# Optimization experiments

Hardware: AMD Instinct MI355X
Metric: run time of the kernel (lower is better)

## Reference

```python
import jax, jax.numpy as jnp
import numpy as np

B = 4; C = 3; IMG = 256; P = 16; HP = 16; HW = 256
DIM = 512; DEPTH = 6; HEADS = 8; DH = 64
NS = 50; SH = 4; SDH = 64; ITERS = 3; RPD = 128; FF = 2048; N = NS + HW


def _ln(x, g, b):
    m = jnp.mean(x, -1, keepdims=True)
    v = jnp.var(x, -1, keepdims=True)
    return (x - m) * jax.lax.rsqrt(v + 1e-5) * g + b


def _rms(x, g):
    # lucidrains RMSNorm: F.normalize(x, dim=-1) * sqrt(dim) * gamma
    n = jnp.linalg.norm(x, axis=-1, keepdims=True)
    return x / jnp.maximum(n, 1e-12) * (DIM ** 0.5) * g


def setup_inputs() -> dict:
    key = jax.random.key(0)
    ks = iter(jax.random.split(key, 64))
    def W(*s):
        return jax.random.normal(next(ks), s, jnp.float32) * 0.02
    SI = SH * SDH
    d = {}
    d['images'] = jax.random.normal(next(ks), (B, C, IMG, IMG), jnp.float32)
    d['slot_noise'] = jax.random.normal(next(ks), (B, NS, DIM), jnp.float32)
    d['patch_w'] = W(C * P * P, DIM); d['patch_b'] = jnp.zeros((DIM,))
    d['hpos'] = W(HP, DIM); d['wpos'] = W(HP, DIM)
    d['rp_w1'] = W(2, RPD); d['rp_b1'] = jnp.zeros((RPD,))
    d['rp_w2'] = W(RPD, RPD); d['rp_b2'] = jnp.zeros((RPD,))
    d['rp_w3'] = W(RPD, HEADS); d['rp_b3'] = jnp.zeros((HEADS,))
    d['slots_mu'] = W(1, 1, DIM); d['slots_logsigma'] = jnp.zeros((1, 1, DIM))
    d['sa_ln_in_g'] = jnp.ones((DIM,)); d['sa_ln_in_b'] = jnp.zeros((DIM,))
    d['sa_ln_sl_g'] = jnp.ones((DIM,)); d['sa_ln_sl_b'] = jnp.zeros((DIM,))
    d['sa_wq'] = W(DIM, SI); d['sa_bq'] = jnp.zeros((SI,))
    d['sa_wk'] = W(DIM, SI); d['sa_bk'] = jnp.zeros((SI,))
    d['sa_wv'] = W(DIM, SI); d['sa_bv'] = jnp.zeros((SI,))
    d['sa_wo'] = W(SI, DIM); d['sa_bo'] = jnp.zeros((DIM,))
    d['gru_wih'] = W(DIM, 3 * DIM); d['gru_whh'] = W(DIM, 3 * DIM)
    d['gru_bih'] = jnp.zeros((3 * DIM,)); d['gru_bhh'] = jnp.zeros((3 * DIM,))
    d['sa_ln_ff_g'] = jnp.ones((DIM,)); d['sa_ln_ff_b'] = jnp.zeros((DIM,))
    d['sa_mlp_w1'] = W(DIM, DIM); d['sa_mlp_b1'] = jnp.zeros((DIM,))
    d['sa_mlp_w2'] = W(DIM, DIM); d['sa_mlp_b2'] = jnp.zeros((DIM,))
    d['s2c_w'] = W(DIM, 2); d['s2c_b'] = jnp.zeros((2,))
    d['attn_g'] = jnp.ones((DEPTH, DIM))
    d['wq'] = W(DEPTH, DIM, HEADS * DH); d['wk'] = W(DEPTH, DIM, HEADS * DH)
    d['wv'] = W(DEPTH, DIM, HEADS * DH); d['wo'] = W(DEPTH, HEADS * DH, DIM)
    d['ff_g'] = jnp.ones((DEPTH, DIM))
    d['ff_w1'] = W(DEPTH, DIM, FF); d['ff_b1'] = jnp.zeros((DEPTH, FF))
    d['ff_w2'] = W(DEPTH, FF, DIM); d['ff_b2'] = jnp.zeros((DEPTH, DIM))
    d['final_g'] = jnp.ones((DIM,))
    d['pred_w'] = W(DIM, DIM); d['pred_b'] = jnp.zeros((DIM,))
    return d


def reference(images, slot_noise, patch_w, patch_b, hpos, wpos,
              rp_w1, rp_b1, rp_w2, rp_b2, rp_w3, rp_b3,
              slots_mu, slots_logsigma, sa_ln_in_g, sa_ln_in_b, sa_ln_sl_g, sa_ln_sl_b,
              sa_wq, sa_bq, sa_wk, sa_bk, sa_wv, sa_bv, sa_wo, sa_bo,
              gru_wih, gru_whh, gru_bih, gru_bhh, sa_ln_ff_g, sa_ln_ff_b,
              sa_mlp_w1, sa_mlp_b1, sa_mlp_w2, sa_mlp_b2, s2c_w, s2c_b,
              attn_g, wq, wk, wv, wo, ff_g, ff_w1, ff_b1, ff_w2, ff_b2,
              final_g, pred_w, pred_b):
    b = images.shape[0]
    # patchify: b c (h p1) (w p2) -> b h w (p1 p2 c)
    x = images.reshape(b, C, HP, P, HP, P).transpose(0, 2, 4, 3, 5, 1).reshape(b, HP, HP, P * P * C)
    tokens = x @ patch_w + patch_b                     # [b, HP, HP, DIM]
    tokens = tokens + hpos[:, None, :] + wpos[None, :, :]
    tokens = tokens.reshape(b, HW, DIM)
    # --- multi-head slot attention ---
    inp = _ln(tokens, sa_ln_in_g, sa_ln_in_b)
    k = (inp @ sa_wk + sa_bk).reshape(b, HW, SH, SDH).transpose(0, 2, 1, 3)
    v = (inp @ sa_wv + sa_bv).reshape(b, HW, SH, SDH).transpose(0, 2, 1, 3)
    slots = slots_mu + jnp.exp(slots_logsigma) * slot_noise  # [b, NS, DIM]
    scale = SDH ** -0.5
    for _ in range(ITERS):
        prev = slots
        s = _ln(slots, sa_ln_sl_g, sa_ln_sl_b)
        q = (s @ sa_wq + sa_bq).reshape(b, NS, SH, SDH).transpose(0, 2, 1, 3)
        dots = jnp.einsum('bhid,bhjd->bhij', q, k) * scale     # [b, SH, NS, HW]
        attn = jax.nn.softmax(dots, axis=-2) + 1e-8            # softmax over slots
        attn = attn / jnp.sum(attn, -1, keepdims=True)         # weighted mean over inputs
        upd = jnp.einsum('bhij,bhjd->bhid', attn, v)
        upd = upd.transpose(0, 2, 1, 3).reshape(b, NS, SH * SDH) @ sa_wo + sa_bo
        # GRUCell(updates, prev_slots)
        gx = upd @ gru_wih + gru_bih
        gh = prev @ gru_whh + gru_bhh
        xr, xz, xn = jnp.split(gx, 3, -1)
        hr, hz, hn = jnp.split(gh, 3, -1)
        r = jax.nn.sigmoid(xr + hr)
        z = jax.nn.sigmoid(xz + hz)
        nn_ = jnp.tanh(xn + r * hn)
        slots = (1 - z) * nn_ + z * prev
        slots = slots + (jax.nn.relu(_ln(slots, sa_ln_ff_g, sa_ln_ff_b) @ sa_mlp_w1 + sa_mlp_b1) @ sa_mlp_w2 + sa_mlp_b2)
    objects = slots
    slot_coords = objects @ s2c_w + s2c_b              # [b, NS, 2]
    # --- relative position MLP bias (slots coords + patch grid) ---
    g = jnp.arange(HP, dtype=jnp.float32)
    grid = jnp.stack(jnp.meshgrid(g, g, indexing='ij'), -1).reshape(HW, 2)
    coords = jnp.concatenate([slot_coords, jnp.broadcast_to(grid, (b, HW, 2))], axis=1)  # [b, N, 2]
    rel = coords[:, :, None, :] - coords[:, None, :, :]   # [b, N, N, 2]
    hmid = jax.nn.silu(rel @ rp_w1 + rp_b1)
    hmid = jax.nn.silu(hmid @ rp_w2 + rp_b2)
    bias = jnp.transpose(hmid @ rp_w3 + rp_b3, (0, 3, 1, 2))  # [b, HEADS, N, N]
    # --- transformer with per-layer rel-pos bias ---
    x = jnp.concatenate([objects, tokens], axis=1)     # [b, N, DIM]
    ascale = DH ** -0.5
    for l in range(DEPTH):
        h = _rms(x, attn_g[l])
        qh = (h @ wq[l]).reshape(b, N, HEADS, DH).transpose(0, 2, 1, 3)
        kh = (h @ wk[l]).reshape(b, N, HEADS, DH).transpose(0, 2, 1, 3)
        vh = (h @ wv[l]).reshape(b, N, HEADS, DH).transpose(0, 2, 1, 3)
        sim = jnp.einsum('bhid,bhjd->bhij', qh, kh) * ascale + bias
        a = jax.nn.softmax(sim, -1)
        o = jnp.einsum('bhij,bhjd->bhid', a, vh).transpose(0, 2, 1, 3).reshape(b, N, HEADS * DH) @ wo[l]
        x = x + o
        h = _rms(x, ff_g[l])
        x = x + (jax.nn.gelu(h @ ff_w1[l] + ff_b1[l]) @ ff_w2[l] + ff_b2[l])
    x = _rms(x, final_g)
    return x[:, NS:] @ pred_w + pred_b                 # [b, HW, DIM]
```

## Files before the change

kernel.cpp:

```cpp
#include <hip/hip_runtime.h>
#include <hip/hip_bf16.h>

typedef __hip_bfloat16 bf16;
typedef short short8v __attribute__((ext_vector_type(8)));
typedef float float4v __attribute__((ext_vector_type(4)));

static __device__ __forceinline__ float b2f(bf16 x){ return __bfloat162float(x); }

static __device__ __forceinline__ float ldin(const void* p, size_t i, bool isbf) {
  return isbf ? b2f(((const bf16*)p)[i]) : ((const float*)p)[i];
}

static __device__ __forceinline__ unsigned short f2bu(float f) {
  bf16 h = __float2bfloat16(f);
  return *reinterpret_cast<unsigned short*>(&h);
}

#define CDIV(a,b) (((a)+(b)-1)/(b))

#define NB   4
#define NSL  50
#define HWT  256
#define NT   306
#define DIM  512
#define NH   8
#define FF   2048
#define RPP  28100
#define PCH  56200

static __device__ __forceinline__ void rp_decode(int q, int& i, int& j) {
  if (q < 15300) { i = q / NT; j = q % NT; }
  else { int r = q - 15300; i = NSL + r / NSL; j = r % NSL; }
}

__global__ void detect_k(const void* p, int* flag) {
  const unsigned short* u = (const unsigned short*)p;
  int t = threadIdx.x;
  int e = (u[t] >> 7) & 0xFF;
  __shared__ int anybad;
  if (t == 0) anybad = 0;
  __syncthreads();
  if (e >= 0x88) atomicOr(&anybad, 1);
  __syncthreads();
  if (t == 0) *flag = anybad ? 0 : 1;
}

struct WtArgs {
  const void* W[17];
  unsigned long long wto[17];
  int K[17], N[17];
  int base[18];
};

__global__ __launch_bounds__(256) void wtrans_all_k(WtArgs a, unsigned short* __restrict__ WT,
                                                    const int* __restrict__ flagp) {
  const bool isbf = *flagp != 0;
  int bid = blockIdx.x;
  int idx = 0;
#pragma unroll
  for (int i = 1; i < 17; ++i) if (bid >= a.base[i]) idx = i;
  int t0 = bid - a.base[idx];
  const int K = a.K[idx], N = a.N[idx];
  const int tilesN = N >> 6;
  const int perLayer = tilesN * (K >> 6);
  const int layer = t0 / perLayer, rem = t0 % perLayer;
  const int n0 = (rem % tilesN) * 64, k0 = (rem / tilesN) * 64;
  const void* W = a.W[idx];
  unsigned short* dst0 = WT + a.wto[idx];
  const size_t slice = (size_t)K * N * layer;

  __shared__ unsigned short S[64 * 72];
  int t = threadIdx.x;
  int kk = t >> 4, nn = (t & 15) * 4;
#pragma unroll
  for (int r = 0; r < 4; ++r) {
    int k = k0 + kk + r * 16;
    unsigned short v[4];
    if (isbf) {
      ushort4 u = *(const ushort4*)((const unsigned short*)W + slice + (size_t)k * N + n0 + nn);
      v[0]=u.x; v[1]=u.y; v[2]=u.z; v[3]=u.w;
    } else {
      float4 f = *(const float4*)((const float*)W + slice + (size_t)k * N + n0 + nn);
      v[0]=f2bu(f.x); v[1]=f2bu(f.y); v[2]=f2bu(f.z); v[3]=f2bu(f.w);
    }
#pragma unroll
    for (int i = 0; i < 4; ++i) S[(nn + i) * 72 + kk + r * 16] = v[i];
  }
  __syncthreads();
  int nr = t >> 2, kc = (t & 3) * 16;
  short8v s0 = *(const short8v*)&S[nr * 72 + kc];
  short8v s1 = *(const short8v*)&S[nr * 72 + kc + 8];
  unsigned short* dst = dst0 + slice + (size_t)(n0 + nr) * K + k0 + kc;
  *(short8v*)dst = s0;
  *(short8v*)(dst + 8) = s1;
}

static __device__ __forceinline__ void gemm_epi(
    float4v accv, int row0, int col,
    const void* __restrict__ bias, size_t boff,
    void* __restrict__ C, int oty,
    int M, int N, int kbeg,
    int act, int mode, int spec,
    const void* __restrict__ p0, const void* __restrict__ p1,
    bool isbf)
{
  float bv = (bias && kbeg == 0) ? ldin(bias, boff + col, isbf) : 0.f;
#pragma unroll
  for (int r = 0; r < 4; ++r) {
    int row = row0 + r;
    if (row >= M) continue;
    float v = accv[r] + bv;
    if (act == 1) v = fmaxf(v, 0.f);
    else if (act == 2) {
      float u = 0.7978845608028654f * (v + 0.044715f * v * v * v);
      v = 0.5f * v * (1.f + tanhf(u));
    } else if (act == 3) {
      v = v / (1.f + expf(-v));
    }
    if (spec == 2 && kbeg == 0) {
      int hh = (row >> 4) & 15, ww = row & 15;
      v += ldin(p0, hh * N + col, isbf) + ldin(p1, ww * N + col, isbf);
    }
    if (spec == 1) {
      int b_ = row / NT, n_ = row % NT;
      if (n_ >= NSL) {
        size_t oi = ((size_t)(b_ * HWT + (n_ - NSL))) * N + col;
        if (isbf) ((bf16*)C)[oi] = __float2bfloat16(v);
        else      ((float*)C)[oi] = v;
      }
    } else {
      size_t idx = (size_t)row * N + col;
      if (oty) ((bf16*)C)[idx] = __float2bfloat16(v);
      else {
        float* Cf = (float*)C;
        if (mode == 2) atomicAdd(&Cf[idx], v);
        else if (mode == 1) Cf[idx] += v;
        else Cf[idx] = v;
      }
    }
  }
}

#define LDK 72
static __device__ __forceinline__ void gemm_body2(
    const void* __restrict__ A, int aty,
    const unsigned short* __restrict__ WT,
    const void* __restrict__ bias, size_t boff,
    void* __restrict__ C, int oty,
    int M, int N, int K, int kbeg, int kend,
    int act, int mode, int spec,
    const void* __restrict__ p0, const void* __restrict__ p1,
    bool isbf)
{
  __shared__ unsigned short As[64 * LDK];
  __shared__ unsigned short Bs[64 * LDK];
  const int tid = threadIdx.x;
  const int lane = tid & 63, wave = tid >> 6;
  const int quad = lane >> 4, ti = lane & 15;
  const int wm = (wave & 1) * 32, wn = (wave >> 1) * 32;
  const int bm = blockIdx.y * 64, bn = blockIdx.x * 64;
  const int srow = tid >> 2, sch = (tid & 3) * 16;

  unsigned short ha[16], hb[16];
  const int gm = bm + srow;
  const bool aok = gm < M;
  const unsigned short* Abf = (const unsigned short*)A + (size_t)gm * K;
  const float*          Af  = (const float*)A + (size_t)gm * K;
  const unsigned short* Bp  = WT + (size_t)(bn + srow) * K;

  auto fetchA = [&](int k0) {
    if (aok) {
      if (aty) {
        const ushort4* ap = (const ushort4*)(Abf + k0 + sch);
#pragma unroll
        for (int i = 0; i < 4; ++i) {
          ushort4 u = ap[i];
          ha[i*4+0]=u.x; ha[i*4+1]=u.y; ha[i*4+2]=u.z; ha[i*4+3]=u.w;
        }
      } else {
        const float4* ap = (const float4*)(Af + k0 + sch);
#pragma unroll
        for (int i = 0; i < 4; ++i) {
          float4 f = ap[i];
          ha[i*4+0]=f2bu(f.x); ha[i*4+1]=f2bu(f.y); ha[i*4+2]=f2bu(f.z); ha[i*4+3]=f2bu(f.w);
        }
      }
    } else {
#pragma unroll
      for (int i = 0; i < 16; ++i) ha[i] = 0;
    }
  };
  auto fetchB = [&](int k0) {
    const ushort4* bp = (const ushort4*)(Bp + k0 + sch);
#pragma unroll
    for (int i = 0; i < 4; ++i) {
      ushort4 u = bp[i];
      hb[i*4+0]=u.x; hb[i*4+1]=u.y; hb[i*4+2]=u.z; hb[i*4+3]=u.w;
    }
  };

  float4v acc00 = {0,0,0,0}, acc01 = {0,0,0,0}, acc10 = {0,0,0,0}, acc11 = {0,0,0,0};
  fetchA(kbeg); fetchB(kbeg);
  for (int k0 = kbeg; k0 < kend; k0 += 64) {
    *(short8v*)&As[srow * LDK + sch]     = *(short8v*)ha;
    *(short8v*)&As[srow * LDK + sch + 8] = *(short8v*)(ha + 8);
    *(short8v*)&Bs[srow * LDK + sch]     = *(short8v*)hb;
    *(short8v*)&Bs[srow * LDK + sch + 8] = *(short8v*)(hb + 8);
    __syncthreads();
    if (k0 + 64 < kend) { fetchA(k0 + 64); fetchB(k0 + 64); }
#pragma unroll
    for (int ks = 0; ks < 2; ++ks) {
      short8v a0 = *reinterpret_cast<const short8v*>(&As[(wm + ti)      * LDK + ks * 32 + quad * 8]);
      short8v a1 = *reinterpret_cast<const short8v*>(&As[(wm + 16 + ti) * LDK + ks * 32 + quad * 8]);
      short8v b0 = *reinterpret_cast<const short8v*>(&Bs[(wn + ti)      * LDK + ks * 32 + quad * 8]);
      short8v b1 = *reinterpret_cast<const short8v*>(&Bs[(wn + 16 + ti) * LDK + ks * 32 + quad * 8]);
      acc00 = __builtin_amdgcn_mfma_f32_16x16x32_bf16(a0, b0, acc00, 0, 0, 0);
      acc01 = __builtin_amdgcn_mfma_f32_16x16x32_bf16(a0, b1, acc01, 0, 0, 0);
      acc10 = __builtin_amdgcn_mfma_f32_16x16x32_bf16(a1, b0, acc10, 0, 0, 0);
      acc11 = __builtin_amdgcn_mfma_f32_16x16x32_bf16(a1, b1, acc11, 0, 0, 0);
    }
    __syncthreads();
  }

  float4v accs[2][2] = {{acc00, acc01}, {acc10, acc11}};
#pragma unroll
  for (int mi = 0; mi < 2; ++mi)
#pragma unroll
    for (int ni = 0; ni < 2; ++ni)
      gemm_epi(accs[mi][ni], bm + wm + mi * 16 + quad * 4, bn + wn + ni * 16 + ti,
               bias, boff, C, oty, M, N, kbeg, act, mode, spec, p0, p1, isbf);
}

__global__ __launch_bounds__(256) void gemm_mfma(
    const void* A, int aty, const unsigned short* WT, size_t woff,
    const void* bias, size_t boff, void* C, int oty,
    int M, int N, int K, int act, int accum, int zsplit,
    int spec, const void* p0, const void* p1, const int* __restrict__ flagp)
{
  int ksz = K / zsplit;
  int kbeg = blockIdx.z * ksz;
  int mode = zsplit > 1 ? 2 : (accum ? 1 : 0);
  gemm_body2(A, aty, WT + woff, bias, boff, C, oty, M, N, K, kbeg, kbeg + ksz,
             act, mode, spec, p0, p1, *flagp != 0);
}

__global__ __launch_bounds__(256) void gemm_mfma_tri(
    const void* A, int aty, const unsigned short* WT, size_t o0, size_t o1, size_t o2,
    void* C0, void* C1, void* C2, int oty, int M, int N, int K,
    const int* __restrict__ flagp)
{
  size_t o = blockIdx.z == 0 ? o0 : (blockIdx.z == 1 ? o1 : o2);
  void* C = blockIdx.z == 0 ? C0 : (blockIdx.z == 1 ? C1 : C2);
  gemm_body2(A, aty, WT + o, nullptr, 0, C, oty, M, N, K, 0, K, 0, 0, 0,
             nullptr, nullptr, *flagp != 0);
}

__global__ __launch_bounds__(256) void gemm_mfma_duo(
    const void* A0, const void* A1, int aty, const unsigned short* WT, size_t o0, size_t o1,
    const void* bias0, const void* bias1, void* C0, void* C1, int oty,
    int M, int N, int K, const int* __restrict__ flagp)
{
  const void* A = blockIdx.z ? A1 : A0;
  size_t o = blockIdx.z ? o1 : o0;
  const void* bias = blockIdx.z ? bias1 : bias0;
  void* C = blockIdx.z ? C1 : C0;
  gemm_body2(A, aty, WT + o, bias, 0, C, oty, M, N, K, 0, K, 0, 0, 0,
             nullptr, nullptr, *flagp != 0);
}

__global__ void coords_k(const float* __restrict__ slots, const void* __restrict__ w,
                         const void* __restrict__ bv, float* __restrict__ coords,
                         const int* __restrict__ flagp) {
  const bool isbf = *flagp != 0;
  __shared__ float r0[256], r1[256];
  int blk = blockIdx.x, t = threadIdx.x;
  if (blk < 200) {
    int b = blk / 50, n = blk % 50;
    const float* x = slots + (size_t)blk * DIM;
    float v0 = x[t], v1 = x[t + 256];
    float a0 = v0 * ldin(w, 2 * t, isbf)     + v1 * ldin(w, 2 * (t + 256), isbf);
    float a1 = v0 * ldin(w, 2 * t + 1, isbf) + v1 * ldin(w, 2 * (t + 256) + 1, isbf);
    r0[t] = a0; r1[t] = a1;
    __syncthreads();
    for (int o = 128; o > 0; o >>= 1) {
      if (t < o) { r0[t] += r0[t + o]; r1[t] += r1[t + o]; }
      __syncthreads();
    }
    if (t == 0) {
      coords[((size_t)b * NT + n) * 2]     = r0[0] + ldin(bv, 0, isbf);
      coords[((size_t)b * NT + n) * 2 + 1] = r1[0] + ldin(bv, 1, isbf);
    }
  } else {
#pragma unroll
    for (int s = 0; s < 4; ++s) {
      int i = t + 256 * s;
      int b = i >> 8, tt = i & 255;
      coords[((size_t)b * NT + NSL + tt) * 2]     = (float)(tt >> 4);
      coords[((size_t)b * NT + NSL + tt) * 2 + 1] = (float)(tt & 15);
    }
  }
}

__global__ void patchify_k(const void* __restrict__ img, unsigned short* __restrict__ xp,
                           const int* __restrict__ flagp) {
  const bool isbf = *flagp != 0;
  int i = blockIdx.x * 256 + threadIdx.x;
  if (i >= NB * HWT * 768) return;
  int col = i % 768, row = i / 768;
  int c = col % 3, p2 = (col / 3) & 15, p1 = col / 48;
  int w = row & 15, h = (row >> 4) & 15, b = row >> 8;
  xp[i] = f2bu(ldin(img, (((size_t)(b * 3 + c) * 256 + h * 16 + p1) * 256) + w * 16 + p2, isbf));
}

__global__ void ln512_k(const float* __restrict__ X, const void* __restrict__ g,
                        const void* __restrict__ b, unsigned short* __restrict__ Y,
                        const int* __restrict__ flagp) {
  const bool isbf = *flagp != 0;
  int row = blockIdx.x, t = threadIdx.x;
  const float* x = X + (size_t)row * DIM;
  float v0 = x[t], v1 = x[t + 256];
  __shared__ float rs[256], rq[256];
  rs[t] = v0 + v1; rq[t] = v0 * v0 + v1 * v1;
  __syncthreads();
  for (int o = 128; o > 0; o >>= 1) {
    if (t < o) { rs[t] += rs[t + o]; rq[t] += rq[t + o]; }
    __syncthreads();
  }
  float mean = rs[0] * (1.f / 512.f);
  float var  = rq[0] * (1.f / 512.f) - mean * mean;
  float inv  = rsqrtf(var + 1e-5f);
  unsigned short* y = Y + (size_t)row * DIM;
  y[t]       = f2bu((v0 - mean) * inv * ldin(g, t, isbf)       + ldin(b, t, isbf));
  y[t + 256] = f2bu((v1 - mean) * inv * ldin(g, t + 256, isbf) + ldin(b, t + 256, isbf));
}

__global__ void rms512_k(const float* __restrict__ X, const void* __restrict__ g,
                         int goff, unsigned short* __restrict__ Y, const int* __restrict__ flagp) {
  const bool isbf = *flagp != 0;
  int row = blockIdx.x, t = threadIdx.x;
  const float* x = X + (size_t)row * DIM;
  float v0 = x[t], v1 = x[t + 256];
  __shared__ float rq[256];
  rq[t] = v0 * v0 + v1 * v1;
  __syncthreads();
  for (int o = 128; o > 0; o >>= 1) {
    if (t < o) rq[t] += rq[t + o];
    __syncthreads();
  }
  float nrm = sqrtf(rq[0]);
  float sc = 22.62741699796952f / fmaxf(nrm, 1e-12f);
  unsigned short* y = Y + (size_t)row * DIM;
  y[t]       = f2bu(v0 * sc * ldin(g, goff + t, isbf));
  y[t + 256] = f2bu(v1 * sc * ldin(g, goff + t + 256, isbf));
}

__global__ void slots_init_k(const void* __restrict__ mu, const void* __restrict__ ls,
                             const void* __restrict__ noise, float* __restrict__ slots,
                             const int* __restrict__ flagp) {
  const bool isbf = *flagp != 0;
  int i = blockIdx.x * 256 + threadIdx.x;
  if (i >= NB * NSL * DIM) return;
  int d = i & 511;
  slots[i] = ldin(mu, d, isbf) + expf(ldin(ls, d, isbf)) * ldin(noise, i, isbf);
}

__global__ void slot_dots_k(const float* __restrict__ q, const float* __restrict__ k,
                            float* __restrict__ dots) {
  int blk = blockIdx.x;
  int i = blk % 50, h = (blk / 50) & 3, b = blk / 200;
  int j = threadIdx.x;
  __shared__ float qs[64];
  if (threadIdx.x < 64) qs[threadIdx.x] = q[((size_t)(b * 50 + i)) * 256 + h * 64 + threadIdx.x];
  __syncthreads();
  const float* kr = k + ((size_t)(b * 256 + j)) * 256 + h * 64;
  float s = 0.f;
#pragma unroll 8
  for (int d = 0; d < 64; ++d) s = fmaf(qs[d], kr[d], s);
  dots[(((size_t)(b * 4 + h) * 50) + i) * 256 + j] = s * 0.125f;
}

__global__ void colsm_k(float* __restrict__ dots) {
  int idx = blockIdx.x * 256 + threadIdx.x;
  if (idx >= 4096) return;
  int j = idx & 255, bh = idx >> 8;
  float* base = dots + ((size_t)bh * NSL) * 256 + j;
  float v[NSL];
#pragma unroll
  for (int i = 0; i < NSL; ++i) v[i] = base[i * 256];
  float m = -1e30f;
#pragma unroll
  for (int i = 0; i < NSL; ++i) m = fmaxf(m, v[i]);
  float s = 0.f;
#pragma unroll
  for (int i = 0; i < NSL; ++i) { float e = __expf(v[i] - m); v[i] = e; s += e; }
  float inv = 1.f / s;
#pragma unroll
  for (int i = 0; i < NSL; ++i) base[i * 256] = fmaf(v[i], inv, 1e-8f);
}

__global__ void slot_upd_k(const float* __restrict__ attn, const float* __restrict__ v,
                           float* __restrict__ upd) {
  int bi = blockIdx.x;
  int b = bi / 50, i = bi % 50;
  int t = threadIdx.x, h = t >> 6, lane = t & 63;
  const float* arow = attn + ((size_t)((b * 4 + h) * 50) + i) * 256;
  float s4 = arow[lane] + arow[lane + 64] + arow[lane + 128] + arow[lane + 192];
#pragma unroll
  for (int o = 1; o < 64; o <<= 1) s4 += __shfl_xor(s4, o);
  float inv = 1.f / s4;
  float s = 0.f;
  for (int j = 0; j < 256; ++j) s = fmaf(arow[j], v[((size_t)(b * 256 + j)) * 256 + t], s);
  upd[(size_t)bi * 256 + t] = s * inv;
}

__global__ __launch_bounds__(256) void gruln_k(
    const float* __restrict__ gx, const float* __restrict__ gh,
    float* __restrict__ slots, const void* __restrict__ g, const void* __restrict__ bb,
    unsigned short* __restrict__ Y, const int* __restrict__ flagp) {
  const bool isbf = *flagp != 0;
  int row = blockIdx.x, t = threadIdx.x;
  size_t b3 = (size_t)row * 1536;
  float s01[2];
#pragma unroll
  for (int half = 0; half < 2; ++half) {
    int d = t + half * 256;
    float xr = gx[b3 + d], xz = gx[b3 + 512 + d], xn = gx[b3 + 1024 + d];
    float hr = gh[b3 + d], hz = gh[b3 + 512 + d], hn = gh[b3 + 1024 + d];
    float r = 1.f / (1.f + expf(-(xr + hr)));
    float z = 1.f / (1.f + expf(-(xz + hz)));
    float n = tanhf(xn + r * hn);
    float prev = slots[(size_t)row * DIM + d];
    s01[half] = (1.f - z) * n + z * prev;
    slots[(size_t)row * DIM + d] = s01[half];
  }
  __shared__ float rs[256], rq[256];
  rs[t] = s01[0] + s01[1];
  rq[t] = s01[0] * s01[0] + s01[1] * s01[1];
  __syncthreads();
  for (int o = 128; o > 0; o >>= 1) {
    if (t < o) { rs[t] += rs[t + o]; rq[t] += rq[t + o]; }
    __syncthreads();
  }
  float mean = rs[0] * (1.f / 512.f);
  float var  = rq[0] * (1.f / 512.f) - mean * mean;
  float inv  = rsqrtf(var + 1e-5f);
  unsigned short* y = Y + (size_t)row * DIM;
  y[t]       = f2bu((s01[0] - mean) * inv * ldin(g, t, isbf)       + ldin(bb, t, isbf));
  y[t + 256] = f2bu((s01[1] - mean) * inv * ldin(g, t + 256, isbf) + ldin(bb, t + 256, isbf));
}

__global__ void relpos_table_k(const void* w1, const void* b1, const void* w2,
                               const void* b2, const void* w3, const void* b3,
                               float* __restrict__ tab, const int* __restrict__ flagp) {
  const bool isbf = *flagp != 0;
  int blk = blockIdx.x;
  float r0 = (float)(blk / 31 - 15), r1 = (float)(blk % 31 - 15);
  int t = threadIdx.x;
  __shared__ float h1[128], h2[128];
  float a = fmaf(r0, ldin(w1, t, isbf), fmaf(r1, ldin(w1, 128 + t, isbf), ldin(b1, t, isbf)));
  h1[t] = a / (1.f + expf(-a));
  __syncthreads();
  float s = ldin(b2, t, isbf);
#pragma unroll 4
  for (int k = 0; k < 128; ++k) s = fmaf(h1[k], ldin(w2, k * 128 + t, isbf), s);
  h2[t] = s / (1.f + expf(-s));
  __syncthreads();
  if (t < 8) {
    float o = ldin(b3, t, isbf);
#pragma unroll 4
    for (int k = 0; k < 128; ++k) o = fmaf(h2[k], ldin(w3, k * 8 + t, isbf), o);
    tab[blk * 8 + t] = o;
  }
}

__global__ void rp_l1_k(const float* __restrict__ coords, const void* w1, const void* b1,
                        unsigned short* __restrict__ H, int pbase, int pcount,
                        const int* __restrict__ flagp) {
  const bool isbf = *flagp != 0;
  int idx = blockIdx.x * 256 + threadIdx.x;
  if (idx >= pcount * 128) return;
  int pl = idx >> 7, u = idx & 127;
  int p = pbase + pl;
  int q = p % RPP, bb = p / RPP;
  int ii, jj;
  rp_decode(q, ii, jj);
  float r0 = coords[(bb * NT + ii) * 2]     - coords[(bb * NT + jj) * 2];
  float r1 = coords[(bb * NT + ii) * 2 + 1] - coords[(bb * NT + jj) * 2 + 1];
  float a = fmaf(r0, ldin(w1, u, isbf), fmaf(r1, ldin(w1, 128 + u, isbf), ldin(b1, u, isbf)));
  H[(size_t)pl * 128 + u] = f2bu(a / (1.f + expf(-a)));
}

__global__ __launch_bounds__(256) void rp_l3_k(
    const unsigned short* __restrict__ H2, const void* w3, const void* b3,
    float* __restrict__ bias, int pbase, int pcount, const int* __restrict__ flagp) {
  const bool isbf = *flagp != 0;
  __shared__ float W3s[8 * 132];
  int t = threadIdx.x;
  for (int e = t; e < 1024; e += 256) {
    int k = e >> 3, hh = e & 7;
    W3s[hh * 132 + k] = ldin(w3, e, isbf);
  }
  __syncthreads();
  int pl = blockIdx.x * 32 + (t >> 3), hh = t & 7;
  if (pl >= pcount) return;
  int p = pbase + pl;
  int q = p % RPP, bb = p / RPP;
  int ii, jj;
  rp_decode(q, ii, jj);
  float s = ldin(b3, hh, isbf);
  const unsigned short* hrow = H2 + (size_t)pl * 128;
  const float* wrow = &W3s[hh * 132];
#pragma unroll 8
  for (int k4 = 0; k4 < 32; ++k4) {
    ushort4 h4 = *(const ushort4*)(hrow + k4 * 4);
    float4  w4 = *(const float4*)(wrow + k4 * 4);
    s = fmaf(b2f(*reinterpret_cast<bf16*>(&h4.x)), w4.x, s);
    s = fmaf(b2f(*reinterpret_cast<bf16*>(&h4.y)), w4.y, s);
    s = fmaf(b2f(*reinterpret_cast<bf16*>(&h4.z)), w4.z, s);
    s = fmaf(b2f(*reinterpret_cast<bf16*>(&h4.w)), w4.w, s);
  }
  bias[((size_t)(bb * NH + hh) * NT + ii) * NT + jj] = s;
}

__global__ void build_x_k(const float* __restrict__ slots, const float* __restrict__ tok,
                          float* __restrict__ x) {
  int i = blockIdx.x * 256 + threadIdx.x;
  if (i >= NB * NT * DIM) return;
  int d = i & 511, n = (i >> 9) % NT, b = i / (NT * DIM);
  x[i] = (n < NSL) ? slots[((size_t)(b * NSL + n)) * DIM + d]
                   : tok[((size_t)(b * HWT + (n - NSL))) * DIM + d];
}

__global__ __launch_bounds__(256) void attn_fused_k(
    const unsigned short* __restrict__ Qb, const unsigned short* __restrict__ Kb,
    const unsigned short* __restrict__ Vb, const float* __restrict__ bias,
    const float* __restrict__ tab, unsigned short* __restrict__ Ob)
{
  const int bh = blockIdx.y, b = bh >> 3, h = bh & 7;
  const int i0 = blockIdx.x * 32;
  __shared__ unsigned short Qs[32 * 72];
  __shared__ unsigned short Ks[64 * 72];
  __shared__ float S[32 * 332];
  __shared__ float TabS[961];
  unsigned short* P = (unsigned short*)S;

  const int tid = threadIdx.x;
  const int lane = tid & 63, wave = tid >> 6, quad = lane >> 4, ti = lane & 15;
  const int mi = wave & 1, nh = wave >> 1;

  for (int e = tid; e < 961; e += 256) TabS[e] = tab[e * 8 + h];

  {
    int r = tid >> 3, c = (tid & 7) * 8;
    int gi = i0 + r;
    ushort4 u0 = {0,0,0,0}, u1 = {0,0,0,0};
    if (gi < NT) {
      const ushort4* p = (const ushort4*)(Qb + ((size_t)(b * NT + gi)) * DIM + h * 64 + c);
      u0 = p[0]; u1 = p[1];
    }
    *(ushort4*)&Qs[r * 72 + c] = u0;
    *(ushort4*)&Qs[r * 72 + c + 4] = u1;
  }

  for (int kt = 0; kt < 5; ++kt) {
    __syncthreads();
    {
      int kr = tid >> 2, c = (tid & 3) * 16;
      int gj = kt * 64 + kr;
      ushort4 v[4] = {{0,0,0,0},{0,0,0,0},{0,0,0,0},{0,0,0,0}};
      if (gj < NT) {
        const ushort4* p = (const ushort4*)(Kb + ((size_t)(b * NT + gj)) * DIM + h * 64 + c);
#pragma unroll
        for (int i = 0; i < 4; ++i) v[i] = p[i];
      }
#pragma unroll
      for (int i = 0; i < 4; ++i) *(ushort4*)&Ks[kr * 72 + c + i * 4] = v[i];
    }
    __syncthreads();
#pragma unroll
    for (int ntl = 0; ntl < 2; ++ntl) {
      int nt = nh * 2 + ntl;
      float4v acc = {0,0,0,0};
#pragma unroll
      for (int ks = 0; ks < 2; ++ks) {
        short8v a  = *(const short8v*)&Qs[(mi * 16 + ti) * 72 + ks * 32 + quad * 8];
        short8v bb = *(const short8v*)&Ks[(nt * 16 + ti) * 72 + ks * 32 + quad * 8];
        acc = __builtin_amdgcn_mfma_f32_16x16x32_bf16(a, bb, acc, 0, 0, 0);
      }
      int colL = kt * 64 + nt * 16 + ti;
      int row0 = mi * 16 + quad * 4;
#pragma unroll
      for (int r = 0; r < 4; ++r) {
        int row_g = i0 + row0 + r;
        float val;
        if (colL < NT) {
          float bv = 0.f;
          if (row_g < NT) {
            if (row_g >= NSL && colL >= NSL) {
              int ii = row_g - NSL, jj = colL - NSL;
              int di = (ii >> 4) - (jj >> 4) + 15;
              int dj = (ii & 15) - (jj & 15) + 15;
              bv = TabS[di * 31 + dj];
            } else {
              bv = bias[((size_t)bh * NT + row_g) * NT + colL];
            }
          }
          val = acc[r] * 0.125f + bv;
        } else val = -1e30f;
        S[(row0 + r) * 332 + colL] = val;
      }
    }
  }
  __syncthreads();

  {
    int rl = tid >> 3, sub = tid & 7;
    float sv[40];
#pragma unroll
    for (int k = 0; k < 40; ++k) sv[k] = S[rl * 332 + sub + k * 8];
    float m = -1e30f;
#pragma unroll
    for (int k = 0; k < 40; ++k) m = fmaxf(m, sv[k]);
    m = fmaxf(m, __shfl_xor(m, 1));
    m = fmaxf(m, __shfl_xor(m, 2));
    m = fmaxf(m, __shfl_xor(m, 4));
    float s = 0.f;
#pragma unroll
    for (int k = 0; k < 40; ++k) { float e = __expf(sv[k] - m); sv[k] = e; s += e; }
    s += __shfl_xor(s, 1);
    s += __shfl_xor(s, 2);
    s += __shfl_xor(s, 4);
    float inv = 1.f / s;
    __syncthreads();
#pragma unroll
    for (int k = 0; k < 40; ++k) P[rl * 664 + sub + k * 8] = f2bu(sv[k] * inv);
  }

  float4v oacc[2] = {{0,0,0,0},{0,0,0,0}};
  for (int vt = 0; vt < 5; ++vt) {
    __syncthreads();
    {
      int key = tid & 63, d0 = (tid >> 6) * 16;
      int gj = vt * 64 + key;
      unsigned short hv[16];
      if (gj < NT) {
        const ushort4* p = (const ushort4*)(Vb + ((size_t)(b * NT + gj)) * DIM + h * 64 + d0);
#pragma unroll
        for (int i = 0; i < 4; ++i) {
          ushort4 u = p[i];
          hv[i*4+0]=u.x; hv[i*4+1]=u.y; hv[i*4+2]=u.z; hv[i*4+3]=u.w;
        }
      } else {
#pragma unroll
        for (int i = 0; i < 16; ++i) hv[i] = 0;
      }
#pragma unroll
      for (int i = 0; i < 16; ++i) Ks[(d0 + i) * 72 + key] = hv[i];
    }
    __syncthreads();
#pragma unroll
    for (int ntl = 0; ntl < 2; ++ntl) {
      int nt = nh * 2 + ntl;
#pragma unroll
      for (int ks = 0; ks < 2; ++ks) {
        short8v a  = *(const short8v*)&P[(mi * 16 + ti) * 664 + vt * 64 + ks * 32 + quad * 8];
        short8v bb = *(const short8v*)&Ks[(nt * 16 + ti) * 72 + ks * 32 + quad * 8];
        oacc[ntl] = __builtin_amdgcn_mfma_f32_16x16x32_bf16(a, bb, oacc[ntl], 0, 0, 0);
      }
    }
  }

#pragma unroll
  for (int ntl = 0; ntl < 2; ++ntl) {
    int dim = nh * 32 + ntl * 16 + ti;
#pragma unroll
    for (int r = 0; r < 4; ++r) {
      int row_g = i0 + mi * 16 + quad * 4 + r;
      if (row_g < NT)
        Ob[((size_t)(b * NT + row_g)) * DIM + h * 64 + dim] = f2bu(oacc[ntl][r]);
    }
  }
}

extern "C" void kernel_launch(void* const* d_in, const int* in_sizes, int n_in,
                              void* d_out, int out_size, void* d_ws, size_t ws_size,
                              hipStream_t stream) {
  const void* images        = d_in[0];
  const void* slot_noise    = d_in[1];
  const void* patch_w       = d_in[2];
  const void* patch_b       = d_in[3];
  const void* hpos          = d_in[4];
  const void* wpos          = d_in[5];
  const void* rp_w1         = d_in[6];
  const void* rp_b1         = d_in[7];
  const void* rp_w2         = d_in[8];
  const void* rp_b2         = d_in[9];
  const void* rp_w3         = d_in[10];
  const void* rp_b3         = d_in[11];
  const void* slots_mu      = d_in[12];
  const void* slots_logsig  = d_in[13];
  const void* sa_ln_in_g    = d_in[14];
  const void* sa_ln_in_b    = d_in[15];
  const void* sa_ln_sl_g    = d_in[16];
  const void* sa_ln_sl_b    = d_in[17];
  const void* sa_wq         = d_in[18];
  const void* sa_bq         = d_in[19];
  const void* sa_wk         = d_in[20];
  const void* sa_bk         = d_in[21];
  const void* sa_wv         = d_in[22];
  const void* sa_bv         = d_in[23];
  const void* sa_wo         = d_in[24];
  const void* sa_bo         = d_in[25];
  const void* gru_wih       = d_in[26];
  const void* gru_whh       = d_in[27];
  const void* gru_bih       = d_in[28];
  const void* gru_bhh       = d_in[29];
  const void* sa_ln_ff_g    = d_in[30];
  const void* sa_ln_ff_b    = d_in[31];
  const void* sa_mlp_w1     = d_in[32];
  const void* sa_mlp_b1     = d_in[33];
  const void* sa_mlp_w2     = d_in[34];
  const void* sa_mlp_b2     = d_in[35];
  const void* s2c_w         = d_in[36];
  const void* s2c_b         = d_in[37];
  const void* attn_g        = d_in[38];
  const void* wq            = d_in[39];
  const void* wk            = d_in[40];
  const void* wv            = d_in[41];
  const void* wo            = d_in[42];
  const void* ff_g          = d_in[43];
  const void* ff_w1         = d_in[44];
  const void* ff_b1         = d_in[45];
  const void* ff_w2         = d_in[46];
  const void* ff_b2         = d_in[47];
  const void* final_g       = d_in[48];
  const void* pred_w        = d_in[49];
  const void* pred_b        = d_in[50];

  float* ws = (float*)d_ws;
  int* FLAG = (int*)ws;
  size_t off = 16;
  auto alloc = [&](size_t n) { float* p = ws + off; off += (n + 15) & ~(size_t)15; return p; };
  float* TOK   = alloc((size_t)NB * HWT * DIM);
  unsigned short* INPB = (unsigned short*)alloc((size_t)NB * HWT * DIM / 2);
  float* KB    = alloc((size_t)NB * HWT * 256);
  float* VB    = alloc((size_t)NB * HWT * 256);
  float* SLOTS = alloc((size_t)NB * NSL * DIM);
  unsigned short* SLNB = (unsigned short*)alloc((size_t)NB * NSL * DIM / 2);
  float* QB    = alloc((size_t)NB * NSL * 256);
  float* ATT   = alloc((size_t)NB * 4 * NSL * HWT);
  float* UPD   = alloc((size_t)NB * NSL * 256);
  float* UPDP  = alloc((size_t)NB * NSL * DIM);
  unsigned short* HIDSB = (unsigned short*)alloc((size_t)NB * NSL * DIM / 2);
  float* CRD   = alloc((size_t)NB * NT * 2);
  float* TAB   = alloc((size_t)961 * 8);
  float* BIAS  = alloc((size_t)NB * NH * NT * NT);
  float* X     = alloc((size_t)NB * NT * DIM);
  unsigned short* HBB  = (unsigned short*)alloc((size_t)NB * NT * DIM / 2);
  unsigned short* QHB  = (unsigned short*)alloc((size_t)NB * NT * DIM / 2);
  unsigned short* KHB  = (unsigned short*)alloc((size_t)NB * NT * DIM / 2);
  unsigned short* VHB  = (unsigned short*)alloc((size_t)NB * NT * DIM / 2);
  float* SIM   = alloc((size_t)NB * NH * NT * NT);
  unsigned short* OBB  = (unsigned short*)alloc((size_t)NB * NT * DIM / 2);
  unsigned short* FFHB = (unsigned short*)alloc((size_t)NB * NT * FF / 2);
  float* OUTT  = alloc((size_t)NB * NT * DIM);
  unsigned short* XPB = (unsigned short*)OUTT;
  float* GX = SIM;
  float* GH = SIM + (size_t)NB * NSL * 1536;
  const size_t oPatch = 0;
  const size_t oKw    = oPatch + (size_t)512 * 768;
  const size_t oVw    = oKw    + (size_t)256 * 512;
  const size_t oQw    = oVw    + (size_t)256 * 512;
  const size_t oWo    = oQw    + (size_t)256 * 512;
  const size_t oGih   = oWo    + (size_t)512 * 256;
  const size_t oGhh   = oGih   + (size_t)1536 * 512;
  const size_t oMlp1  = oGhh   + (size_t)1536 * 512;
  const size_t oMlp2  = oMlp1  + (size_t)512 * 512;
  const size_t oRp2   = oMlp2  + (size_t)512 * 512;
  const size_t oWq    = oRp2   + (size_t)128 * 128;
  const size_t oWk    = oWq    + (size_t)6 * 512 * 512;
  const size_t oWv    = oWk    + (size_t)6 * 512 * 512;
  const size_t oWol   = oWv    + (size_t)6 * 512 * 512;
  const size_t oFf1   = oWol   + (size_t)6 * 512 * 512;
  const size_t oFf2   = oFf1   + (size_t)6 * 512 * 2048;
  const size_t oPred  = oFf2   + (size_t)6 * 2048 * 512;
  const size_t wtTotal = oPred + (size_t)512 * 512;
  unsigned short* WTS = (unsigned short*)alloc((wtTotal + 1) / 2);
  (void)ws_size; (void)in_sizes; (void)n_in; (void)out_size;

#define GEMMM(A_, ATY_, WOFF_, BIAS_, BOFF_, C_, OTY_, M_, N_, K_, ACT_, ACC_, ZS_, SPEC_, P0_, P1_) \
  gemm_mfma<<<dim3((N_)/64, CDIV((M_),64), (ZS_)), 256, 0, stream>>>( \
      A_, ATY_, WTS, (size_t)(WOFF_), BIAS_, (size_t)(BOFF_), C_, OTY_, M_, N_, K_, ACT_, ACC_, ZS_, \
      SPEC_, P0_, P1_, FLAG)

  const int MROW = NB * NT;
  const int MS   = NB * NSL;

  detect_k<<<1, 256, 0, stream>>>(images, FLAG);
  {
    WtArgs a;
    const void* Wp[17] = { patch_w, sa_wk, sa_wv, sa_wq, sa_wo, gru_wih, gru_whh,
                           sa_mlp_w1, sa_mlp_w2, rp_w2, wq, wk, wv, wo, ff_w1, ff_w2, pred_w };
    const size_t Oo[17] = { oPatch, oKw, oVw, oQw, oWo, oGih, oGhh,
                            oMlp1, oMlp2, oRp2, oWq, oWk, oWv, oWol, oFf1, oFf2, oPred };
    const int Kk[17] = {768,512,512,512,256,512,512,512,512,128,512,512,512,512,512,2048,512};
    const int Nn[17] = {512,256,256,256,512,1536,1536,512,512,128,512,512,512,512,2048,512,512};
    const int Ll[17] = {1,1,1,1,1,1,1,1,1,1,6,6,6,6,6,6,1};
    int acc = 0;
    for (int i = 0; i < 17; ++i) {
      a.W[i] = Wp[i]; a.wto[i] = Oo[i]; a.K[i] = Kk[i]; a.N[i] = Nn[i];
      a.base[i] = acc;
      acc += Ll[i] * (Kk[i] >> 6) * (Nn[i] >> 6);
    }
    a.base[17] = acc;
    wtrans_all_k<<<acc, 256, 0, stream>>>(a, WTS, FLAG);
  }

  patchify_k<<<CDIV(NB*HWT*768, 256), 256, 0, stream>>>(images, XPB, FLAG);
  hipMemsetAsync(TOK, 0, (size_t)NB * HWT * DIM * sizeof(float), stream);
  GEMMM(XPB, 1, oPatch, patch_b, 0, TOK, 0, NB*HWT, DIM, 768, 0, 0, 3, 2, hpos, wpos);

  ln512_k<<<NB*HWT, 256, 0, stream>>>(TOK, sa_ln_in_g, sa_ln_in_b, INPB, FLAG);
  gemm_mfma_duo<<<dim3(4, 16, 2), 256, 0, stream>>>(
      INPB, INPB, 1, WTS, oKw, oVw, sa_bk, sa_bv, KB, VB, 0, NB*HWT, 256, DIM, FLAG);
  slots_init_k<<<CDIV(NB*NSL*DIM, 256), 256, 0, stream>>>(slots_mu, slots_logsig, slot_noise, SLOTS, FLAG);

  for (int it = 0; it < 3; ++it) {
    ln512_k<<<MS, 256, 0, stream>>>(SLOTS, sa_ln_sl_g, sa_ln_sl_b, SLNB, FLAG);
    GEMMM(SLNB, 1, oQw, sa_bq, 0, QB, 0, MS, 256, DIM, 0, 0, 1, 0, nullptr, nullptr);
    slot_dots_k<<<NB*4*NSL, 256, 0, stream>>>(QB, KB, ATT);
    colsm_k<<<16, 256, 0, stream>>>(ATT);
    slot_upd_k<<<MS, 256, 0, stream>>>(ATT, VB, UPD);
    GEMMM(UPD, 0, oWo, sa_bo, 0, UPDP, 0, MS, DIM, 256, 0, 0, 1, 0, nullptr, nullptr);
    gemm_mfma_duo<<<dim3(24, 4, 2), 256, 0, stream>>>(
        UPDP, SLOTS, 0, WTS, oGih, oGhh, gru_bih, gru_bhh, GX, GH, 0, MS, 1536, DIM, FLAG);
    gruln_k<<<MS, 256, 0, stream>>>(GX, GH, SLOTS, sa_ln_ff_g, sa_ln_ff_b, SLNB, FLAG);
    GEMMM(SLNB, 1, oMlp1, sa_mlp_b1, 0, HIDSB, 1, MS, DIM, DIM, 1, 0, 1, 0, nullptr, nullptr);
    GEMMM(HIDSB, 1, oMlp2, sa_mlp_b2, 0, SLOTS, 0, MS, DIM, DIM, 0, 1, 1, 0, nullptr, nullptr);
  }

  coords_k<<<201, 256, 0, stream>>>(SLOTS, s2c_w, s2c_b, CRD, FLAG);
  relpos_table_k<<<961, 128, 0, stream>>>(rp_w1, rp_b1, rp_w2, rp_b2, rp_w3, rp_b3, TAB, FLAG);
  {
    unsigned short* H1 = HBB;
    unsigned short* H2 = HBB + (size_t)PCH * 128;
    for (int c = 0; c < 2; ++c) {
      int pb = c * PCH;
      rp_l1_k<<<CDIV(PCH*128, 256), 256, 0, stream>>>(CRD, rp_w1, rp_b1, H1, pb, PCH, FLAG);
      GEMMM(H1, 1, oRp2, rp_b2, 0, H2, 1, PCH, 128, 128, 3, 0, 1, 0, nullptr, nullptr);
      rp_l3_k<<<CDIV(PCH,32), 256, 0, stream>>>(H2, rp_w3, rp_b3, BIAS, pb, PCH, FLAG);
    }
  }

  build_x_k<<<CDIV(NB*NT*DIM, 256), 256, 0, stream>>>(SLOTS, TOK, X);
  for (int l = 0; l < 6; ++l) {
    size_t lw = (size_t)l * 512 * 512;
    rms512_k<<<MROW, 256, 0, stream>>>(X, attn_g, l * DIM, HBB, FLAG);
    gemm_mfma_tri<<<dim3(8, 20, 3), 256, 0, stream>>>(
        HBB, 1, WTS, oWq + lw, oWk + lw, oWv + lw, QHB, KHB, VHB, 1, MROW, DIM, DIM, FLAG);
    attn_fused_k<<<dim3(10, NB*NH), 256, 0, stream>>>(QHB, KHB, VHB, BIAS, TAB, OBB);
    GEMMM(OBB, 1, oWol + lw, (const void*)nullptr, 0, X, 0, MROW, DIM, DIM, 0, 1, 2, 0, nullptr, nullptr);
    rms512_k<<<MROW, 256, 0, stream>>>(X, ff_g, l * DIM, HBB, FLAG);
    GEMMM(HBB, 1, oFf1 + (size_t)l * 512 * 2048, ff_b1, l * FF, FFHB, 1, MROW, FF, DIM, 2, 0, 1, 0, nullptr, nullptr);
    GEMMM(FFHB, 1, oFf2 + (size_t)l * 2048 * 512, ff_b2, l * DIM, X, 0, MROW, DIM, FF, 0, 1, 4, 0, nullptr, nullptr);
  }

  rms512_k<<<MROW, 256, 0, stream>>>(X, final_g, 0, HBB, FLAG);
  GEMMM(HBB, 1, oPred, pred_b, 0, d_out, 0, MROW, DIM, DIM, 0, 0, 1, 1, nullptr, nullptr);

#undef GEMMM
}
```

Baseline: 1.158 ms.

## Merge small prep kernels, unchunk relpos MLP, trim pred GEMM rows

Patchify and slot init now run as one launch, and so do the coords and relpos-table kernels. The two-chunk relpos MLP becomes a single pass using dedicated H1/H2 buffers. The weight-transpose kernel processes 128-wide K tiles per block, and the final prediction GEMM computes only the 1024 token rows by remapping A rows instead of all rows. Together these cut launch count and skip slot-row work in the output projection, at the cost of extra buffer memory and bigger transpose tiles.

```diff
diff --git a/kernel.cpp b/kernel.cpp
--- a/kernel.cpp
+++ b/kernel.cpp
@@ -26,7 +26,7 @@
 #define NH   8
 #define FF   2048
 #define RPP  28100
-#define PCH  56200
+#define NPR  (NB*RPP)
 
 static __device__ __forceinline__ void rp_decode(int q, int& i, int& j) {
   if (q < 15300) { i = q / NT; j = q % NT; }
@@ -62,18 +62,18 @@
   int t0 = bid - a.base[idx];
   const int K = a.K[idx], N = a.N[idx];
   const int tilesN = N >> 6;
-  const int perLayer = tilesN * (K >> 6);
+  const int perLayer = tilesN * (K >> 7);
   const int layer = t0 / perLayer, rem = t0 % perLayer;
-  const int n0 = (rem % tilesN) * 64, k0 = (rem / tilesN) * 64;
+  const int n0 = (rem % tilesN) * 64, k0 = (rem / tilesN) * 128;
   const void* W = a.W[idx];
   unsigned short* dst0 = WT + a.wto[idx];
   const size_t slice = (size_t)K * N * layer;
 
-  __shared__ unsigned short S[64 * 72];
+  __shared__ unsigned short S[64 * 136];
   int t = threadIdx.x;
   int kk = t >> 4, nn = (t & 15) * 4;
 #pragma unroll
-  for (int r = 0; r < 4; ++r) {
+  for (int r = 0; r < 8; ++r) {
     int k = k0 + kk + r * 16;
     unsigned short v[4];
     if (isbf) {
@@ -84,15 +84,14 @@
       v[0]=f2bu(f.x); v[1]=f2bu(f.y); v[2]=f2bu(f.z); v[3]=f2bu(f.w);
     }
 #pragma unroll
-    for (int i = 0; i < 4; ++i) S[(nn + i) * 72 + kk + r * 16] = v[i];
+    for (int i = 0; i < 4; ++i) S[(nn + i) * 136 + kk + r * 16] = v[i];
   }
   __syncthreads();
-  int nr = t >> 2, kc = (t & 3) * 16;
-  short8v s0 = *(const short8v*)&S[nr * 72 + kc];
-  short8v s1 = *(const short8v*)&S[nr * 72 + kc + 8];
+  int nr = t >> 2, kc = (t & 3) * 32;
   unsigned short* dst = dst0 + slice + (size_t)(n0 + nr) * K + k0 + kc;
-  *(short8v*)dst = s0;
-  *(short8v*)(dst + 8) = s1;
+#pragma unroll
+  for (int i = 0; i < 4; ++i)
+    *(short8v*)(dst + i * 8) = *(const short8v*)&S[nr * 136 + kc + i * 8];
 }
 
 static __device__ __forceinline__ void gemm_epi(
@@ -128,6 +127,10 @@
         if (isbf) ((bf16*)C)[oi] = __float2bfloat16(v);
         else      ((float*)C)[oi] = v;
       }
+    } else if (spec == 3) {
+      size_t oi = (size_t)row * N + col;
+      if (isbf) ((bf16*)C)[oi] = __float2bfloat16(v);
+      else      ((float*)C)[oi] = v;
     } else {
       size_t idx = (size_t)row * N + col;
       if (oty) ((bf16*)C)[idx] = __float2bfloat16(v);
@@ -164,8 +167,10 @@
   unsigned short ha[16], hb[16];
   const int gm = bm + srow;
   const bool aok = gm < M;
-  const unsigned short* Abf = (const unsigned short*)A + (size_t)gm * K;
-  const float*          Af  = (const float*)A + (size_t)gm * K;
+  int arow = gm;
+  if (spec == 3) arow = ((gm >> 8) * NT) + NSL + (gm & 255);
+  const unsigned short* Abf = (const unsigned short*)A + (size_t)arow * K;
+  const float*          Af  = (const float*)A + (size_t)arow * K;
   const unsigned short* Bp  = WT + (size_t)(bn + srow) * K;
 
   auto fetchA = [&](int k0) {
@@ -268,11 +273,16 @@
              nullptr, nullptr, *flagp != 0);
 }
 
-__global__ void coords_k(const float* __restrict__ slots, const void* __restrict__ w,
-                         const void* __restrict__ bv, float* __restrict__ coords,
-                         const int* __restrict__ flagp) {
+__global__ __launch_bounds__(256) void coords_table_k(
+    const float* __restrict__ slots, const void* __restrict__ w,
+    const void* __restrict__ bv,
+    const void* w1, const void* b1, const void* w2, const void* b2,
+    const void* w3, const void* b3,
+    float* __restrict__ coords, float* __restrict__ tab,
+    const int* __restrict__ flagp) {
   const bool isbf = *flagp != 0;
   __shared__ float r0[256], r1[256];
+  __shared__ float h1[128], h2[128];
   int blk = blockIdx.x, t = threadIdx.x;
   if (blk < 200) {
     int b = blk / 50, n = blk % 50;
@@ -290,7 +300,7 @@
       coords[((size_t)b * NT + n) * 2]     = r0[0] + ldin(bv, 0, isbf);
       coords[((size_t)b * NT + n) * 2 + 1] = r1[0] + ldin(bv, 1, isbf);
     }
-  } else {
+  } else if (blk == 200) {
 #pragma unroll
     for (int s = 0; s < 4; ++s) {
       int i = t + 256 * s;
@@ -298,18 +308,47 @@
       coords[((size_t)b * NT + NSL + tt) * 2]     = (float)(tt >> 4);
       coords[((size_t)b * NT + NSL + tt) * 2 + 1] = (float)(tt & 15);
     }
-  }
-}
-
-__global__ void patchify_k(const void* __restrict__ img, unsigned short* __restrict__ xp,
-                           const int* __restrict__ flagp) {
+  } else {
+    int e = blk - 201;
+    float rr0 = (float)(e / 31 - 15), rr1 = (float)(e % 31 - 15);
+    if (t < 128) {
+      float a = fmaf(rr0, ldin(w1, t, isbf), fmaf(rr1, ldin(w1, 128 + t, isbf), ldin(b1, t, isbf)));
+      h1[t] = a / (1.f + expf(-a));
+    }
+    __syncthreads();
+    if (t < 128) {
+      float s = ldin(b2, t, isbf);
+#pragma unroll 4
+      for (int k = 0; k < 128; ++k) s = fmaf(h1[k], ldin(w2, k * 128 + t, isbf), s);
+      h2[t] = s / (1.f + expf(-s));
+    }
+    __syncthreads();
+    if (t < 8) {
+      float o = ldin(b3, t, isbf);
+#pragma unroll 4
+      for (int k = 0; k < 128; ++k) o = fmaf(h2[k], ldin(w3, k * 8 + t, isbf), o);
+      tab[e * 8 + t] = o;
+    }
+  }
+}
+
+__global__ void prep_k(const void* __restrict__ img, unsigned short* __restrict__ xp,
+                       const void* __restrict__ mu, const void* __restrict__ ls,
+                       const void* __restrict__ noise, float* __restrict__ slots,
+                       const int* __restrict__ flagp) {
   const bool isbf = *flagp != 0;
-  int i = blockIdx.x * 256 + threadIdx.x;
-  if (i >= NB * HWT * 768) return;
-  int col = i % 768, row = i / 768;
-  int c = col % 3, p2 = (col / 3) & 15, p1 = col / 48;
-  int w = row & 15, h = (row >> 4) & 15, b = row >> 8;
-  xp[i] = f2bu(ldin(img, (((size_t)(b * 3 + c) * 256 + h * 16 + p1) * 256) + w * 16 + p2, isbf));
+  int blk = blockIdx.x;
+  if (blk < 3072) {
+    int i = blk * 256 + threadIdx.x;
+    int col = i % 768, row = i / 768;
+    int c = col % 3, p2 = (col / 3) & 15, p1 = col / 48;
+    int w = row & 15, h = (row >> 4) & 15, b = row >> 8;
+    xp[i] = f2bu(ldin(img, (((size_t)(b * 3 + c) * 256 + h * 16 + p1) * 256) + w * 16 + p2, isbf));
+  } else {
+    int i = (blk - 3072) * 256 + threadIdx.x;
+    int d = i & 511;
+    slots[i] = ldin(mu, d, isbf) + expf(ldin(ls, d, isbf)) * ldin(noise, i, isbf);
+  }
 }
 
 __global__ void ln512_k(const float* __restrict__ X, const void* __restrict__ g,
@@ -352,16 +391,6 @@
   unsigned short* y = Y + (size_t)row * DIM;
   y[t]       = f2bu(v0 * sc * ldin(g, goff + t, isbf));
   y[t + 256] = f2bu(v1 * sc * ldin(g, goff + t + 256, isbf));
-}
-
-__global__ void slots_init_k(const void* __restrict__ mu, const void* __restrict__ ls,
-                             const void* __restrict__ noise, float* __restrict__ slots,
-                             const int* __restrict__ flagp) {
-  const bool isbf = *flagp != 0;
-  int i = blockIdx.x * 256 + threadIdx.x;
-  if (i >= NB * NSL * DIM) return;
-  int d = i & 511;
-  slots[i] = ldin(mu, d, isbf) + expf(ldin(ls, d, isbf)) * ldin(noise, i, isbf);
 }
 
 __global__ void slot_dots_k(const float* __restrict__ q, const float* __restrict__ k,
@@ -447,30 +476,6 @@
   unsigned short* y = Y + (size_t)row * DIM;
   y[t]       = f2bu((s01[0] - mean) * inv * ldin(g, t, isbf)       + ldin(bb, t, isbf));
   y[t + 256] = f2bu((s01[1] - mean) * inv * ldin(g, t + 256, isbf) + ldin(bb, t + 256, isbf));
-}
-
-__global__ void relpos_table_k(const void* w1, const void* b1, const void* w2,
-                               const void* b2, const void* w3, const void* b3,
-                               float* __restrict__ tab, const int* __restrict__ flagp) {
-  const bool isbf = *flagp != 0;
-  int blk = blockIdx.x;
-  float r0 = (float)(blk / 31 - 15), r1 = (float)(blk % 31 - 15);
-  int t = threadIdx.x;
-  __shared__ float h1[128], h2[128];
-  float a = fmaf(r0, ldin(w1, t, isbf), fmaf(r1, ldin(w1, 128 + t, isbf), ldin(b1, t, isbf)));
-  h1[t] = a / (1.f + expf(-a));
-  __syncthreads();
-  float s = ldin(b2, t, isbf);
-#pragma unroll 4
-  for (int k = 0; k < 128; ++k) s = fmaf(h1[k], ldin(w2, k * 128 + t, isbf), s);
-  h2[t] = s / (1.f + expf(-s));
-  __syncthreads();
-  if (t < 8) {
-    float o = ldin(b3, t, isbf);
-#pragma unroll 4
-    for (int k = 0; k < 128; ++k) o = fmaf(h2[k], ldin(w3, k * 8 + t, isbf), o);
-    tab[blk * 8 + t] = o;
-  }
 }
 
 __global__ void rp_l1_k(const float* __restrict__ coords, const void* w1, const void* b1,
@@ -764,6 +769,8 @@
   unsigned short* OBB  = (unsigned short*)alloc((size_t)NB * NT * DIM / 2);
   unsigned short* FFHB = (unsigned short*)alloc((size_t)NB * NT * FF / 2);
   float* OUTT  = alloc((size_t)NB * NT * DIM);
+  unsigned short* H1 = (unsigned short*)alloc((size_t)NPR * 64);
+  unsigned short* H2 = (unsigned short*)alloc((size_t)NPR * 64);
   unsigned short* XPB = (unsigned short*)OUTT;
   float* GX = SIM;
   float* GH = SIM + (size_t)NB * NSL * 1536;
@@ -797,6 +804,7 @@
   const int MS   = NB * NSL;
 
   detect_k<<<1, 256, 0, stream>>>(images, FLAG);
+  prep_k<<<3472, 256, 0, stream>>>(images, XPB, slots_mu, slots_logsig, slot_noise, SLOTS, FLAG);
   {
     WtArgs a;
     const void* Wp[17] = { patch_w, sa_wk, sa_wv, sa_wq, sa_wo, gru_wih, gru_whh,
@@ -810,20 +818,18 @@
     for (int i = 0; i < 17; ++i) {
       a.W[i] = Wp[i]; a.wto[i] = Oo[i]; a.K[i] = Kk[i]; a.N[i] = Nn[i];
       a.base[i] = acc;
-      acc += Ll[i] * (Kk[i] >> 6) * (Nn[i] >> 6);
+      acc += Ll[i] * (Kk[i] >> 7) * (Nn[i] >> 6);
     }
     a.base[17] = acc;
     wtrans_all_k<<<acc, 256, 0, stream>>>(a, WTS, FLAG);
   }
 
-  patchify_k<<<CDIV(NB*HWT*768, 256), 256, 0, stream>>>(images, XPB, FLAG);
   hipMemsetAsync(TOK, 0, (size_t)NB * HWT * DIM * sizeof(float), stream);
   GEMMM(XPB, 1, oPatch, patch_b, 0, TOK, 0, NB*HWT, DIM, 768, 0, 0, 3, 2, hpos, wpos);
 
   ln512_k<<<NB*HWT, 256, 0, stream>>>(TOK, sa_ln_in_g, sa_ln_in_b, INPB, FLAG);
   gemm_mfma_duo<<<dim3(4, 16, 2), 256, 0, stream>>>(
       INPB, INPB, 1, WTS, oKw, oVw, sa_bk, sa_bv, KB, VB, 0, NB*HWT, 256, DIM, FLAG);
-  slots_init_k<<<CDIV(NB*NSL*DIM, 256), 256, 0, stream>>>(slots_mu, slots_logsig, slot_noise, SLOTS, FLAG);
 
   for (int it = 0; it < 3; ++it) {
     ln512_k<<<MS, 256, 0, stream>>>(SLOTS, sa_ln_sl_g, sa_ln_sl_b, SLNB, FLAG);
@@ -839,18 +845,11 @@
     GEMMM(HIDSB, 1, oMlp2, sa_mlp_b2, 0, SLOTS, 0, MS, DIM, DIM, 0, 1, 1, 0, nullptr, nullptr);
   }
 
-  coords_k<<<201, 256, 0, stream>>>(SLOTS, s2c_w, s2c_b, CRD, FLAG);
-  relpos_table_k<<<961, 128, 0, stream>>>(rp_w1, rp_b1, rp_w2, rp_b2, rp_w3, rp_b3, TAB, FLAG);
-  {
-    unsigned short* H1 = HBB;
-    unsigned short* H2 = HBB + (size_t)PCH * 128;
-    for (int c = 0; c < 2; ++c) {
-      int pb = c * PCH;
-      rp_l1_k<<<CDIV(PCH*128, 256), 256, 0, stream>>>(CRD, rp_w1, rp_b1, H1, pb, PCH, FLAG);
-      GEMMM(H1, 1, oRp2, rp_b2, 0, H2, 1, PCH, 128, 128, 3, 0, 1, 0, nullptr, nullptr);
-      rp_l3_k<<<CDIV(PCH,32), 256, 0, stream>>>(H2, rp_w3, rp_b3, BIAS, pb, PCH, FLAG);
-    }
-  }
+  coords_table_k<<<1162, 256, 0, stream>>>(SLOTS, s2c_w, s2c_b,
+      rp_w1, rp_b1, rp_w2, rp_b2, rp_w3, rp_b3, CRD, TAB, FLAG);
+  rp_l1_k<<<CDIV(NPR*128, 256), 256, 0, stream>>>(CRD, rp_w1, rp_b1, H1, 0, NPR, FLAG);
+  GEMMM(H1, 1, oRp2, rp_b2, 0, H2, 1, NPR, 128, 128, 3, 0, 1, 0, nullptr, nullptr);
+  rp_l3_k<<<CDIV(NPR,32), 256, 0, stream>>>(H2, rp_w3, rp_b3, BIAS, 0, NPR, FLAG);
 
   build_x_k<<<CDIV(NB*NT*DIM, 256), 256, 0, stream>>>(SLOTS, TOK, X);
   for (int l = 0; l < 6; ++l) {
@@ -866,7 +865,7 @@
   }
 
   rms512_k<<<MROW, 256, 0, stream>>>(X, final_g, 0, HBB, FLAG);
-  GEMMM(HBB, 1, oPred, pred_b, 0, d_out, 0, MROW, DIM, DIM, 0, 0, 1, 1, nullptr, nullptr);
+  GEMMM(HBB, 1, oPred, pred_b, 0, d_out, 0, 1024, DIM, DIM, 0, 0, 1, 3, nullptr, nullptr);
 
 #undef GEMMM
 }
```

New measurement: 1.167 ms. No clear change (+0.8%).
